# Performance work log

Measured on AMD Instinct MI355X. Metric: run time of the kernel, lower is better.

## Reference

```python
import jax, jax.numpy as jnp
import numpy as np

IMG_H, IMG_W = 16, 16
N = IMG_H * IMG_W              # 256 tokens
HEADS = 8
HEAD_DIM = 32
INNER = HEADS * HEAD_DIM       # 256
IN_CH = 256
OUT_CH = 256
BATCH = 64
SCALE = HEAD_DIM ** -0.5


def _make_relative_index():
    # Mirrors the torch buffer construction exactly.
    coords = np.stack(np.meshgrid(np.arange(IMG_H), np.arange(IMG_W), indexing='ij'))
    coords = coords.reshape(2, -1)                      # (2, N)
    rel = coords[:, :, None] - coords[:, None, :]       # (2, N, N)
    rel[0] += IMG_H - 1
    rel[1] += IMG_W - 1
    rel[0] *= 2 * IMG_W - 1
    idx = rel.sum(0).reshape(-1)                        # (N*N,) values in [0, (2H-1)(2W-1))
    return idx.astype(np.int32)


def setup_inputs() -> dict:
    key = jax.random.key(0)
    k1, k2, k3, k4, k5 = jax.random.split(key, 5)
    x = jax.random.normal(k1, (BATCH, N, IN_CH), dtype=jnp.float32)
    w_qkv = jax.random.normal(k2, (IN_CH, 3 * INNER), dtype=jnp.float32) * 0.02
    bias_table = jax.random.normal(k3, ((2 * IMG_H - 1) * (2 * IMG_W - 1), HEADS), dtype=jnp.float32) * 0.02
    w_out = jax.random.normal(k4, (INNER, OUT_CH), dtype=jnp.float32) * 0.02
    b_out = jax.random.normal(k5, (OUT_CH,), dtype=jnp.float32) * 0.02
    rel_index = jnp.asarray(_make_relative_index())
    return {"x": x, "w_qkv": w_qkv, "bias_table": bias_table,
            "w_out": w_out, "b_out": b_out, "rel_index": rel_index}


def reference(x, w_qkv, bias_table, w_out, b_out, rel_index):
    b, n, _ = x.shape
    qkv = x @ w_qkv                                     # (b, n, 3*inner)
    q, k, v = jnp.split(qkv, 3, axis=-1)
    def heads(t):
        return t.reshape(b, n, HEADS, HEAD_DIM).transpose(0, 2, 1, 3)  # (b, h, n, d)
    q, k, v = heads(q), heads(k), heads(v)
    dots = jnp.einsum('bhid,bhjd->bhij', q, k) * SCALE  # (b, h, n, n)
    # gather relative position bias: (n*n, h) -> (1, h, n, n)
    rel_bias = bias_table[rel_index].reshape(n, n, HEADS).transpose(2, 0, 1)[None]
    attn = jax.nn.softmax(dots + rel_bias, axis=-1)
    out = jnp.einsum('bhij,bhjd->bhid', attn, v)        # (b, h, n, d)
    out = out.transpose(0, 2, 1, 3).reshape(b, n, INNER)
    return out @ w_out + b_out
```

## Files before the change

### kernel.cpp

```cpp
#include <hip/hip_runtime.h>
#include <hip/hip_bf16.h>

typedef __bf16 bfv8 __attribute__((ext_vector_type(8)));
typedef float f32x4 __attribute__((ext_vector_type(4)));
typedef unsigned short u16;
typedef unsigned int u32;
typedef u16 u16x8 __attribute__((ext_vector_type(8)));

__device__ __forceinline__ float bf2f(u16 u){ union{u32 i; float f;} x; x.i=(u32)u<<16; return x.f; }
__device__ __forceinline__ u16 f2bf(float f){ union{float f; u32 i;} x; x.f=f; u32 i=x.i; return (u16)((i + 0x7FFFu + ((i>>16)&1u))>>16); }

__device__ __forceinline__ void gl16(const void* g, void* l){
  __builtin_amdgcn_global_load_lds((const __attribute__((address_space(1))) unsigned int*)g,
                                   (__attribute__((address_space(3))) unsigned int*)l, 16, 0, 0);
}

__global__ __launch_bounds__(256) void prep_k(const float* __restrict__ x, u16* __restrict__ xb,
                                              const float* __restrict__ w_qkv, u16* __restrict__ wT,
                                              const float* __restrict__ w_out, u16* __restrict__ woT,
                                              const float* __restrict__ bt, const int* __restrict__ ridx,
                                              u16* __restrict__ biasp2){
  __shared__ u16 tile[32][34];
  const int bid = blockIdx.x, tid = threadIdx.x;
  if (bid < 2048){
    int i = (bid*256 + tid)*8;
    float4 a = *(const float4*)&x[i];
    float4 b = *(const float4*)&x[i+4];
    u16 r[8] = { f2bf(a.x),f2bf(a.y),f2bf(a.z),f2bf(a.w), f2bf(b.x),f2bf(b.y),f2bf(b.z),f2bf(b.w) };
    *(int4*)&xb[i] = *(int4*)r;
  } else if (bid < 2048+192){
    int b2 = bid - 2048;
    int c0 = (b2 % 24)*32, r0 = (b2/24)*32;
    int tx = tid & 31, ty = tid >> 5;
    #pragma unroll
    for(int dy=0; dy<32; dy+=8) tile[ty+dy][tx] = f2bf(w_qkv[(size_t)(r0+ty+dy)*768 + (c0+tx)]);
    __syncthreads();
    #pragma unroll
    for(int dy=0; dy<32; dy+=8) wT[(size_t)(c0+ty+dy)*256 + (r0+tx)] = tile[tx][ty+dy];
  } else if (bid < 2048+192+64){
    int b3 = bid - (2048+192);
    int c0 = (b3 & 7)*32, r0 = (b3 >> 3)*32;
    int tx = tid & 31, ty = tid >> 5;
    #pragma unroll
    for(int dy=0; dy<32; dy+=8) tile[ty+dy][tx] = f2bf(w_out[(size_t)(r0+ty+dy)*256 + (c0+tx)]);
    __syncthreads();
    #pragma unroll
    for(int dy=0; dy<32; dy+=8) woT[(size_t)(c0+ty+dy)*256 + (r0+tx)] = tile[tx][ty+dy];
  } else {
    const float L2E = 1.4426950408889634f;
    int idx = (bid - (2048+192+64))*256 + tid;
    int e = idx & 7, ch = (idx>>3)&7, lane = (idx>>6)&63, rb = (idx>>12)&15, h = (idx>>16)&7;
    int ll = lane & 15, lg = lane >> 4;
    int tj = ch*2 + (e>>2), r = e & 3;
    int q = rb*16 + ll, k = 16*tj + 4*lg + r;
    biasp2[idx] = f2bf(bt[ridx[q*256 + k]*8 + h] * L2E);
  }
}

template<bool BIAS, typename OUT, int TM>
__global__ __launch_bounds__(256) void gemm_k(const u16* __restrict__ A, const u16* __restrict__ Bt,
                         const float* __restrict__ bias, OUT* __restrict__ C, int M, int N, int K){
  constexpr int MI = TM/32;
  __shared__ u16 As[TM*64];
  __shared__ u16 Bs[128*64];
  const int tid = threadIdx.x, lane = tid & 63, wv = tid >> 6;
  const int lg = lane >> 4, ll = lane & 15;
  const int wr = (wv >> 1)*(TM/2), wc = (wv & 1)*64;
  const size_t m0 = (size_t)blockIdx.x*TM;
  const int n0 = blockIdx.y*128;
  const int lrow = lane >> 3, lcol = (lane & 7)*8;
  f32x4 acc[MI][4] = {};
  for(int k0=0; k0<K; k0+=64){
    #pragma unroll
    for(int c=0;c<MI;++c){
      int rowbase = (wv*MI + c)*8;
      gl16(&A[(m0 + rowbase + lrow)*(size_t)K + k0 + lcol], &As[rowbase*64]);
    }
    #pragma unroll
    for(int c=0;c<4;++c){
      int rowbase = (wv*4 + c)*8;
      gl16(&Bt[(size_t)(n0 + rowbase + lrow)*K + k0 + lcol], &Bs[rowbase*64]);
    }
    __syncthreads();
    bfv8 af[MI][2], bf[4][2];
    #pragma unroll
    for(int i=0;i<MI;++i)
      #pragma unroll
      for(int kh=0;kh<2;++kh) af[i][kh] = *(const bfv8*)&As[(wr+16*i+ll)*64 + kh*32 + lg*8];
    #pragma unroll
    for(int j=0;j<4;++j)
      #pragma unroll
      for(int kh=0;kh<2;++kh) bf[j][kh] = *(const bfv8*)&Bs[(wc+16*j+ll)*64 + kh*32 + lg*8];
    #pragma unroll
    for(int kh=0;kh<2;++kh)
      #pragma unroll
      for(int i=0;i<MI;++i)
        #pragma unroll
        for(int j=0;j<4;++j)
          acc[i][j] = __builtin_amdgcn_mfma_f32_16x16x32_bf16(af[i][kh], bf[j][kh], acc[i][j], 0,0,0);
    __syncthreads();
  }
  #pragma unroll
  for(int i=0;i<MI;++i)
    #pragma unroll
    for(int j=0;j<4;++j){
      int col = n0 + wc + 16*j + ll;
      float bv = 0.f;
      if (BIAS) bv = bias[col];
      #pragma unroll
      for(int r=0;r<4;++r){
        size_t row = m0 + wr + 16*i + lg*4 + r;
        float v = acc[i][j][r] + bv;
        if constexpr (sizeof(OUT) == 2) C[row*(size_t)N + col] = f2bf(v);
        else                            C[row*(size_t)N + col] = v;
      }
    }
}

__global__ __launch_bounds__(512) void attn_k(const u16* __restrict__ qkv, const u16* __restrict__ biasp2, u16* __restrict__ attnb){
  __shared__ u16 Ks[256*40];
  __shared__ u16 Vt[32*264];
  const int i = blockIdx.x;
  const int b = i & 63, h = i >> 6;
  const int tid = threadIdx.x, lane = tid & 63, wv = tid >> 6;
  const int lg = lane >> 4, ll = lane & 15;
  const u16* qb = qkv + (size_t)b*256*768;
  #pragma unroll
  for(int p=0;p<2;++p){
    int ch = tid + p*512;
    int j = ch >> 2, d8 = (ch & 3)*8;
    *(int4*)&Ks[j*40 + d8] = *(const int4*)&qb[(size_t)j*768 + 256 + h*32 + d8];
  }
  #pragma unroll
  for(int it=0; it<8; ++it){
    int e = tid + it*512;
    int j = e >> 4, dp = (e & 15)*2;
    int jp = ((j>>5)<<5) + 8*((j>>2)&3) + 4*((j>>4)&1) + (j&3);
    u32 v = *(const u32*)&qb[(size_t)j*768 + 512 + h*32 + dp];
    Vt[dp*264 + jp]     = (u16)(v & 0xffffu);
    Vt[(dp+1)*264 + jp] = (u16)(v >> 16);
  }
  __syncthreads();
  const float SCALE2 = 0.17677669529663687f * 1.4426950408889634f;
  const f32x4 zero = {0.f,0.f,0.f,0.f};
  #pragma unroll 1
  for(int iter=0; iter<2; ++iter){
    const int q0 = iter*128 + wv*16;
    const u16* bp = biasp2 + ((((size_t)h*16 + (q0>>4))*64 + lane) << 6);
    u16x8 bias[8];
    #pragma unroll
    for(int g=0; g<8; ++g) bias[g] = *(const u16x8*)&bp[g*8];
    bfv8 qf = *(const bfv8*)&qb[(size_t)(q0+ll)*768 + h*32 + lg*8];
    f32x4 s[16];
    #pragma unroll
    for(int tj=0;tj<16;++tj){
      bfv8 kf = *(const bfv8*)&Ks[(16*tj+ll)*40 + lg*8];
      s[tj] = __builtin_amdgcn_mfma_f32_16x16x32_bf16(kf, qf, zero, 0,0,0);
    }
    f32x4 sm = {0.f,0.f,0.f,0.f};
    #pragma unroll
    for(int tj=0;tj<16;++tj){
      #pragma unroll
      for(int r=0;r<4;++r){
        float p = exp2f(fmaf(s[tj][r], SCALE2, bf2f(bias[tj>>1][4*(tj&1)+r])));
        s[tj][r] = p;
        sm[r] += p;
      }
    }
    float sum = sm[0]+sm[1]+sm[2]+sm[3];
    sum += __shfl_xor(sum,16);
    sum += __shfl_xor(sum,32);
    float rinv = 1.0f/sum;
    u32 pk[16][2];
    #pragma unroll
    for(int tj=0;tj<16;++tj){
      asm("v_cvt_pk_bf16_f32 %0, %1, %2" : "=v"(pk[tj][0]) : "v"(s[tj][0]), "v"(s[tj][1]));
      asm("v_cvt_pk_bf16_f32 %0, %1, %2" : "=v"(pk[tj][1]) : "v"(s[tj][2]), "v"(s[tj][3]));
    }
    f32x4 o[2] = {zero, zero};
    #pragma unroll
    for(int c=0;c<8;++c){
      union { u32 u[4]; bfv8 v; } pu;
      pu.u[0] = pk[2*c][0]; pu.u[1] = pk[2*c][1]; pu.u[2] = pk[2*c+1][0]; pu.u[3] = pk[2*c+1][1];
      bfv8 pf = pu.v;
      #pragma unroll
      for(int td=0;td<2;++td){
        bfv8 vf = *(const bfv8*)&Vt[(16*td+ll)*264 + 32*c + lg*8];
        o[td] = __builtin_amdgcn_mfma_f32_16x16x32_bf16(pf, vf, o[td], 0,0,0);
      }
    }
    #pragma unroll
    for(int td=0;td<2;++td)
      #pragma unroll
      for(int r=0;r<4;++r){
        float rl = __shfl(rinv, 4*lg + r);
        int row = q0 + 4*lg + r;
        attnb[((size_t)b*256 + row)*256 + h*32 + 16*td + ll] = f2bf(o[td][r]*rl);
      }
  }
}

extern "C" void kernel_launch(void* const* d_in, const int* in_sizes, int n_in,
                              void* d_out, int out_size, void* d_ws, size_t ws_size,
                              hipStream_t stream) {
  const float* x     = (const float*)d_in[0];
  const float* w_qkv = (const float*)d_in[1];
  const float* btab  = (const float*)d_in[2];
  const float* w_out = (const float*)d_in[3];
  const float* b_out = (const float*)d_in[4];
  const int*   ridx  = (const int*)d_in[5];
  float* out = (float*)d_out;

  char* ws = (char*)d_ws;
  size_t off = 0;
  u16*   xb     = (u16*)(ws + off); off += (size_t)64*256*256*2;
  u16*   wT     = (u16*)(ws + off); off += (size_t)768*256*2;
  u16*   woT    = (u16*)(ws + off); off += (size_t)256*256*2;
  u16*   biasp2 = (u16*)(ws + off); off += (size_t)524288*2;
  u16*   qkvb   = (u16*)(ws + off); off += (size_t)64*256*768*2;
  u16*   attnb  = (u16*)(ws + off); off += (size_t)64*256*256*2;

  prep_k<<<2048+192+64+2048,256,0,stream>>>(x, xb, w_qkv, wT, w_out, woT, btab, ridx, biasp2);
  gemm_k<false,u16,128><<<dim3(128,6),256,0,stream>>>(xb, wT, nullptr, qkvb, 16384, 768, 256);
  attn_k<<<512,512,0,stream>>>(qkvb, biasp2, attnb);
  gemm_k<true,float,64><<<dim3(256,2),256,0,stream>>>(attnb, woT, b_out, out, 16384, 256, 256);
}
```

Baseline: 58.45 us.

## Stream softmax per key chunk in attention and shrink GEMM M tiles

The attention kernel stops holding all 16 score tiles and bias registers at once. It now computes scores, exp, bf16 packing and the PV MFMA chunk by chunk, and adds a launch_bounds occupancy hint. This lowers register pressure so more waves can be resident and latency is hidden better. Separately, both GEMMs use smaller M tiles and twice as many blocks to fill more CUs, which lowers per-block reuse.

Result: slower. 59.96 us (+2.6%).

```diff
diff --git a/kernel.cpp b/kernel.cpp
--- a/kernel.cpp
+++ b/kernel.cpp
@@ -117,7 +117,7 @@
     }
 }
 
-__global__ __launch_bounds__(512) void attn_k(const u16* __restrict__ qkv, const u16* __restrict__ biasp2, u16* __restrict__ attnb){
+__global__ __launch_bounds__(512,8) void attn_k(const u16* __restrict__ qkv, const u16* __restrict__ biasp2, u16* __restrict__ attnb){
   __shared__ u16 Ks[256*40];
   __shared__ u16 Vt[32*264];
   const int i = blockIdx.x;
@@ -147,56 +147,43 @@
   for(int iter=0; iter<2; ++iter){
     const int q0 = iter*128 + wv*16;
     const u16* bp = biasp2 + ((((size_t)h*16 + (q0>>4))*64 + lane) << 6);
-    u16x8 bias[8];
-    #pragma unroll
-    for(int g=0; g<8; ++g) bias[g] = *(const u16x8*)&bp[g*8];
     bfv8 qf = *(const bfv8*)&qb[(size_t)(q0+ll)*768 + h*32 + lg*8];
-    f32x4 s[16];
-    #pragma unroll
-    for(int tj=0;tj<16;++tj){
-      bfv8 kf = *(const bfv8*)&Ks[(16*tj+ll)*40 + lg*8];
-      s[tj] = __builtin_amdgcn_mfma_f32_16x16x32_bf16(kf, qf, zero, 0,0,0);
-    }
-    f32x4 sm = {0.f,0.f,0.f,0.f};
-    #pragma unroll
-    for(int tj=0;tj<16;++tj){
+    float sum = 0.f;
+    f32x4 o0 = zero, o1 = zero;
+    #pragma unroll
+    for(int c=0;c<8;++c){
+      u16x8 bc = *(const u16x8*)&bp[c*8];
+      bfv8 kf0 = *(const bfv8*)&Ks[(16*(2*c)+ll)*40 + lg*8];
+      bfv8 kf1 = *(const bfv8*)&Ks[(16*(2*c+1)+ll)*40 + lg*8];
+      f32x4 s0 = __builtin_amdgcn_mfma_f32_16x16x32_bf16(kf0, qf, zero, 0,0,0);
+      f32x4 s1 = __builtin_amdgcn_mfma_f32_16x16x32_bf16(kf1, qf, zero, 0,0,0);
+      f32x4 p0, p1;
       #pragma unroll
       for(int r=0;r<4;++r){
-        float p = exp2f(fmaf(s[tj][r], SCALE2, bf2f(bias[tj>>1][4*(tj&1)+r])));
-        s[tj][r] = p;
-        sm[r] += p;
+        p0[r] = exp2f(fmaf(s0[r], SCALE2, bf2f(bc[r])));
+        p1[r] = exp2f(fmaf(s1[r], SCALE2, bf2f(bc[4+r])));
       }
-    }
-    float sum = sm[0]+sm[1]+sm[2]+sm[3];
+      sum += (p0[0]+p0[1]+p0[2]+p0[3]) + (p1[0]+p1[1]+p1[2]+p1[3]);
+      union { u32 u[4]; bfv8 v; } pu;
+      asm("v_cvt_pk_bf16_f32 %0, %1, %2" : "=v"(pu.u[0]) : "v"(p0[0]), "v"(p0[1]));
+      asm("v_cvt_pk_bf16_f32 %0, %1, %2" : "=v"(pu.u[1]) : "v"(p0[2]), "v"(p0[3]));
+      asm("v_cvt_pk_bf16_f32 %0, %1, %2" : "=v"(pu.u[2]) : "v"(p1[0]), "v"(p1[1]));
+      asm("v_cvt_pk_bf16_f32 %0, %1, %2" : "=v"(pu.u[3]) : "v"(p1[2]), "v"(p1[3]));
+      bfv8 vf0 = *(const bfv8*)&Vt[(ll)*264      + 32*c + lg*8];
+      bfv8 vf1 = *(const bfv8*)&Vt[(16+ll)*264   + 32*c + lg*8];
+      o0 = __builtin_amdgcn_mfma_f32_16x16x32_bf16(pu.v, vf0, o0, 0,0,0);
+      o1 = __builtin_amdgcn_mfma_f32_16x16x32_bf16(pu.v, vf1, o1, 0,0,0);
+    }
     sum += __shfl_xor(sum,16);
     sum += __shfl_xor(sum,32);
     float rinv = 1.0f/sum;
-    u32 pk[16][2];
-    #pragma unroll
-    for(int tj=0;tj<16;++tj){
-      asm("v_cvt_pk_bf16_f32 %0, %1, %2" : "=v"(pk[tj][0]) : "v"(s[tj][0]), "v"(s[tj][1]));
-      asm("v_cvt_pk_bf16_f32 %0, %1, %2" : "=v"(pk[tj][1]) : "v"(s[tj][2]), "v"(s[tj][3]));
-    }
-    f32x4 o[2] = {zero, zero};
-    #pragma unroll
-    for(int c=0;c<8;++c){
-      union { u32 u[4]; bfv8 v; } pu;
-      pu.u[0] = pk[2*c][0]; pu.u[1] = pk[2*c][1]; pu.u[2] = pk[2*c+1][0]; pu.u[3] = pk[2*c+1][1];
-      bfv8 pf = pu.v;
-      #pragma unroll
-      for(int td=0;td<2;++td){
-        bfv8 vf = *(const bfv8*)&Vt[(16*td+ll)*264 + 32*c + lg*8];
-        o[td] = __builtin_amdgcn_mfma_f32_16x16x32_bf16(pf, vf, o[td], 0,0,0);
-      }
-    }
-    #pragma unroll
-    for(int td=0;td<2;++td)
-      #pragma unroll
-      for(int r=0;r<4;++r){
-        float rl = __shfl(rinv, 4*lg + r);
-        int row = q0 + 4*lg + r;
-        attnb[((size_t)b*256 + row)*256 + h*32 + 16*td + ll] = f2bf(o[td][r]*rl);
-      }
+    #pragma unroll
+    for(int r=0;r<4;++r){
+      float rl = __shfl(rinv, 4*lg + r);
+      int row = q0 + 4*lg + r;
+      attnb[((size_t)b*256 + row)*256 + h*32 + ll]      = f2bf(o0[r]*rl);
+      attnb[((size_t)b*256 + row)*256 + h*32 + 16 + ll] = f2bf(o1[r]*rl);
+    }
   }
 }
 
@@ -221,7 +208,7 @@
   u16*   attnb  = (u16*)(ws + off); off += (size_t)64*256*256*2;
 
   prep_k<<<2048+192+64+2048,256,0,stream>>>(x, xb, w_qkv, wT, w_out, woT, btab, ridx, biasp2);
-  gemm_k<false,u16,128><<<dim3(128,6),256,0,stream>>>(xb, wT, nullptr, qkvb, 16384, 768, 256);
+  gemm_k<false,u16,64><<<dim3(256,6),256,0,stream>>>(xb, wT, nullptr, qkvb, 16384, 768, 256);
   attn_k<<<512,512,0,stream>>>(qkvb, biasp2, attnb);
-  gemm_k<true,float,64><<<dim3(256,2),256,0,stream>>>(attnb, woT, b_out, out, 16384, 256, 256);
-}
+  gemm_k<true,float,32><<<dim3(512,2),256,0,stream>>>(attnb, woT, b_out, out, 16384, 256, 256);
+}
```
